# Kernel tuning notes

Hardware: AMD Instinct MI355X
Metric: run time of the kernel (lower is better)

## Reference

```python
import jax, jax.numpy as jnp
import numpy as np

EPS = 1e-5

def conv3x3(x, w, b, stride=1):
    y = jax.lax.conv_general_dilated(x, w, (stride, stride), 'SAME',
                                     dimension_numbers=('NCHW', 'OIHW', 'NCHW'))
    return y + b[None, :, None, None]

def batchnorm_train(x, gamma, beta):
    # training-mode BN: batch statistics over (N, H, W)
    mean = x.mean(axis=(0, 2, 3), keepdims=True)
    var = x.var(axis=(0, 2, 3), keepdims=True)
    xh = (x - mean) * jax.lax.rsqrt(var + EPS)
    return xh * gamma[None, :, None, None] + beta[None, :, None, None]

def haar_dwt2(x):
    # pywt.dwt2(x, 'db1') on last two axes; even H,W so 'symmetric' padding is a no-op.
    # a = (x0 + x1)/sqrt2, d = (x0 - x1)/sqrt2 per axis -> 2x2 block combinations / 2.
    x00 = x[:, :, 0::2, 0::2]
    x01 = x[:, :, 0::2, 1::2]
    x10 = x[:, :, 1::2, 0::2]
    x11 = x[:, :, 1::2, 1::2]
    cA = (x00 + x01 + x10 + x11) * 0.5
    cH = (x00 + x01 - x10 - x11) * 0.5  # pywt 'da': detail along rows
    cV = (x00 - x01 + x10 - x11) * 0.5  # pywt 'ad': detail along cols
    cD = (x00 - x01 - x10 + x11) * 0.5
    return cA, cH, cV, cD


def setup_inputs() -> dict:
    key = jax.random.key(0)
    ks = jax.random.split(key, 8)
    N, in_c, out_c, H, W = 4, 3, 64, 512, 512

    def kaiming(k, shape):
        fan_in = shape[1] * shape[2] * shape[3]
        return jax.random.normal(k, shape, jnp.float32) * np.sqrt(2.0 / fan_in)

    inputs = jax.random.normal(ks[0], (N, in_c, H, W), jnp.float32)
    return {
        'inputs': inputs,
        # conv_block: conv1 -> bn1 -> conv2 -> bn2 -> relu
        'w1': kaiming(ks[1], (out_c, in_c, 3, 3)),
        'b1': jnp.zeros((out_c,), jnp.float32),
        'g1': jnp.ones((out_c,), jnp.float32),
        'be1': jnp.zeros((out_c,), jnp.float32),
        'w2': kaiming(ks[2], (out_c, out_c, 3, 3)),
        'b2': jnp.zeros((out_c,), jnp.float32),
        'g2': jnp.ones((out_c,), jnp.float32),
        'be2': jnp.zeros((out_c,), jnp.float32),
        # conv_dwt_block: conv(out_c*4 -> out_c) -> bn -> relu
        'w3': kaiming(ks[3], (out_c, out_c * 4, 3, 3)),
        'b3': jnp.zeros((out_c,), jnp.float32),
        'g3': jnp.ones((out_c,), jnp.float32),
        'be3': jnp.zeros((out_c,), jnp.float32),
    }


def reference(inputs, w1, b1, g1, be1, w2, b2, g2, be2, w3, b3, g3, be3):
    # conv_block
    x = conv3x3(inputs, w1, b1)
    x = batchnorm_train(x, g1, be1)
    x = conv3x3(x, w2, b2)
    x = batchnorm_train(x, g2, be2)
    skip_con = jax.nn.relu(x)

    # original detaches skip_con before the (CPU pywt) DWT -> no grad through this branch
    dwt_in = jax.lax.stop_gradient(skip_con)
    cA, cH, cV, cD = haar_dwt2(dwt_in)
    dwt = jnp.concatenate((cA, cH, cV, cD), axis=1)  # [N, 4*out_c, H/2, W/2]

    y = conv3x3(dwt, w3, b3)
    y = batchnorm_train(y, g3, be3)
    dwt_out = jax.nn.relu(y)
    return dwt_out, skip_con
```

## Files before the change

### kernel.cpp

```cpp
#include <hip/hip_runtime.h>
#include <cstdint>

typedef float f32x4 __attribute__((ext_vector_type(4)));
typedef __bf16 bf16x8 __attribute__((ext_vector_type(8)));
typedef unsigned int uint32;
typedef unsigned short ushort_t;

__device__ __forceinline__ ushort_t f2bf(float f) {
    uint32 u = __builtin_bit_cast(uint32, f);
    u = (u + 0x7fffu + ((u >> 16) & 1u)) >> 16;
    return (ushort_t)u;
}
__device__ __forceinline__ float bf2f(ushort_t h) {
    return __builtin_bit_cast(float, (uint32)h << 16);
}

__global__ __launch_bounds__(256) void im2col1_kernel(
    const float* __restrict__ in,
    ushort_t* __restrict__ P)
{
    int px = blockIdx.x * 256 + threadIdx.x;
    int n = px >> 18, rem = px & 262143;
    int y = rem >> 9, x = rem & 511;
    ushort_t pv[32];
#pragma unroll
    for (int ci = 0; ci < 3; ++ci)
#pragma unroll
        for (int t = 0; t < 9; ++t) {
            int dy = t / 3 - 1, dx = t % 3 - 1;
            int yy = y + dy, xx = x + dx;
            bool v = ((unsigned)yy < 512u) && ((unsigned)xx < 512u);
            pv[ci * 9 + t] = v ? f2bf(in[((n * 3 + ci) * 512 + yy) * 512 + xx])
                               : (ushort_t)0;
        }
#pragma unroll
    for (int k = 27; k < 32; ++k) pv[k] = 0;
    uint4* dst = (uint4*)(P + (size_t)px * 32);
    dst[0] = *(uint4*)(pv);
    dst[1] = *(uint4*)(pv + 8);
    dst[2] = *(uint4*)(pv + 16);
    dst[3] = *(uint4*)(pv + 24);
}

__global__ void prepw1_kernel(const float* __restrict__ w1,
                              ushort_t* __restrict__ Wsw1)
{
    int i = blockIdx.x * 256 + threadIdx.x;
    int ii = i & 7, lane = (i >> 3) & 63, nt = i >> 9;
    int cout = nt * 16 + (lane & 15);
    int k = (lane >> 4) * 8 + ii;
    Wsw1[i] = (k < 27) ? f2bf(w1[cout * 27 + k]) : (ushort_t)0;
}

__global__ __launch_bounds__(256) void gemm1_kernel(
    const ushort_t* __restrict__ P,
    const ushort_t* __restrict__ Wsw1,
    const float* __restrict__ b1,
    ushort_t* __restrict__ X1,
    float* __restrict__ stats)
{
    __shared__ float sred[4][128];
    int tid = threadIdx.x;
    int wave = tid >> 6, lane = tid & 63;
    int lp = lane & 15, lg = lane >> 4;
    int pxb = blockIdx.x * 256 + wave * 64;

    bf16x8 wf[4];
#pragma unroll
    for (int nt = 0; nt < 4; ++nt)
        wf[nt] = *(const bf16x8*)(Wsw1 + (nt * 64 + lane) * 8);

    f32x4 acc[4][4];
#pragma unroll
    for (int a = 0; a < 4; ++a)
#pragma unroll
        for (int b = 0; b < 4; ++b) acc[a][b] = (f32x4){0.f, 0.f, 0.f, 0.f};

#pragma unroll
    for (int nf = 0; nf < 4; ++nf) {
        bf16x8 bfrag = *(const bf16x8*)(P + (size_t)(pxb + nf * 16 + lp) * 32 + lg * 8);
#pragma unroll
        for (int nt = 0; nt < 4; ++nt)
            acc[nt][nf] = __builtin_amdgcn_mfma_f32_16x16x32_bf16(
                wf[nt], bfrag, acc[nt][nf], 0, 0, 0);
    }

    float s16[16], q16[16];
#pragma unroll
    for (int j = 0; j < 16; ++j) { s16[j] = 0.f; q16[j] = 0.f; }

#pragma unroll
    for (int nf = 0; nf < 4; ++nf) {
        size_t px = (size_t)pxb + nf * 16 + lp;
#pragma unroll
        for (int nt = 0; nt < 4; ++nt) {
            ushort_t ov[4];
#pragma unroll
            for (int r = 0; r < 4; ++r) {
                float o = acc[nt][nf][r] + b1[nt * 16 + lg * 4 + r];
                s16[nt * 4 + r] += o;
                q16[nt * 4 + r] += o * o;
                ov[r] = f2bf(o);
            }
            *(ushort4*)(X1 + px * 64 + nt * 16 + lg * 4) = *(ushort4*)ov;
        }
    }

#pragma unroll
    for (int off = 1; off < 16; off <<= 1)
#pragma unroll
        for (int j = 0; j < 16; ++j) {
            s16[j] += __shfl_xor(s16[j], off);
            q16[j] += __shfl_xor(q16[j], off);
        }
    if (lp == 0) {
#pragma unroll
        for (int nt = 0; nt < 4; ++nt)
#pragma unroll
            for (int r = 0; r < 4; ++r) {
                int ch = nt * 16 + lg * 4 + r;
                sred[wave][ch]      = s16[nt * 4 + r];
                sred[wave][64 + ch] = q16[nt * 4 + r];
            }
    }
    __syncthreads();
    if (tid < 128) {
        float tot = sred[0][tid] + sred[1][tid] + sred[2][tid] + sred[3][tid];
        atomicAdd(&stats[(blockIdx.x & 31) * 128 + tid], tot);
    }
}

__global__ void finalize_kernel(const float* __restrict__ stats,
                                const float* __restrict__ gamma,
                                const float* __restrict__ beta,
                                float inv_cnt, float* __restrict__ scsh)
{
    int c = threadIdx.x;
    float S = 0.f, Q = 0.f;
    for (int b = 0; b < 32; ++b) {
        S += stats[b * 128 + c];
        Q += stats[b * 128 + 64 + c];
    }
    float mean = S * inv_cnt;
    float var  = Q * inv_cnt - mean * mean;
    float rs   = rsqrtf(var + 1e-5f);
    float sc   = gamma[c] * rs;
    scsh[c]      = sc;
    scsh[64 + c] = beta[c] - mean * sc;
}

__global__ __launch_bounds__(256) void prepw_kernel(
    const float* __restrict__ w, const float* __restrict__ scale,
    ushort_t* __restrict__ Wsw, int CIN)
{
    int i = blockIdx.x * 256 + threadIdx.x;
    int KC = CIN >> 5;
    int ii = i & 7, lane = (i >> 3) & 63, nt = (i >> 9) & 3;
    int rest = i >> 11;
    int kc = rest % KC, t = rest / KC;
    if (t >= 9) return;
    int cout = nt * 16 + (lane & 15);
    int cin  = kc * 32 + (lane >> 4) * 8 + ii;
    float v = w[(cout * CIN + cin) * 9 + t];
    if (scale) v *= scale[cin];
    Wsw[i] = f2bf(v);
}

__global__ void prepT_kernel(const float* __restrict__ w2,
                             const float* __restrict__ shift,
                             float* __restrict__ T)
{
    int idx = threadIdx.x;
    if (idx < 576) {
        int t = idx / 64, cout = idx % 64;
        float s = 0.f;
        for (int cin = 0; cin < 64; ++cin)
            s += w2[(cout * 64 + cin) * 9 + t] * shift[cin];
        T[idx] = s;
    }
    __syncthreads();
    if (idx < 64) {
        float s = 0.f;
        for (int t = 0; t < 9; ++t) s += T[t * 64 + idx];
        T[576 + idx] = s;
    }
}

template <int CIN, bool HAS_T, int HH, int WW>
__global__ __launch_bounds__(256, 4) void conv_mfma4_kernel(
    const ushort_t* __restrict__ X,
    const ushort_t* __restrict__ Wsw,
    const float* __restrict__ T,
    const float* __restrict__ bias,
    ushort_t* __restrict__ Y,
    float* __restrict__ stats)
{
    constexpr int KC     = CIN >> 5;
    constexpr int COLS_B = WW >> 6;
    constexpr int ROWS_B = HH >> 2;

    __shared__ ushort_t tile[12672];
    __shared__ float sred[4][128];

    int nwg = gridDim.x;
    int bid = blockIdx.x;
    int cpx = nwg >> 3;
    int bs  = (bid & 7) * cpx + (bid >> 3);

    int tid  = threadIdx.x;
    int wave = tid >> 6, lane = tid & 63;
    int lp = lane & 15, lg = lane >> 4;

    int tmp = bs;
    int ctile = tmp % COLS_B;  tmp /= COLS_B;
    int rtile = tmp % ROWS_B;
    int n     = tmp / ROWS_B;
    int y0 = rtile << 2, x0 = ctile << 6;
    int y  = y0 + wave;

    f32x4 acc[4][4];
#pragma unroll
    for (int a = 0; a < 4; ++a)
#pragma unroll
        for (int b = 0; b < 4; ++b) acc[a][b] = (f32x4){0.f, 0.f, 0.f, 0.f};

#pragma unroll 1
    for (int c = 0; c < KC; ++c) {
        if (c) __syncthreads();
#pragma unroll
        for (int j = 0; j < 7; ++j) {
            int s = tid + j * 256;
            if (s < 1584) {
                int px = s >> 2, cb = s & 3;
                int ry = px / 66, cx = px - ry * 66;
                int gy = y0 - 1 + ry, gx = x0 - 1 + cx;
                uint4 v = {0u, 0u, 0u, 0u};
                if (((unsigned)gy < (unsigned)HH) && ((unsigned)gx < (unsigned)WW))
                    v = *(const uint4*)(X + ((size_t)(n * HH + gy) * WW + gx) * CIN
                                          + c * 32 + cb * 8);
                *(uint4*)(tile + cb * 3168 + px * 8) = v;
            }
        }
        __syncthreads();

#pragma unroll
        for (int t = 0; t < 9; ++t) {
            const int dy = t / 3 - 1, dx = t % 3 - 1;
            bf16x8 wf[4];
#pragma unroll
            for (int nt = 0; nt < 4; ++nt)
                wf[nt] = *(const bf16x8*)(Wsw + (size_t)(((t * KC + c) << 2) + nt) * 512 + lane * 8);
            int prow = (wave + 1 + dy) * 66 + (1 + dx) + lp;
#pragma unroll
            for (int nf = 0; nf < 4; ++nf) {
                int px = prow + nf * 16;
                bf16x8 bfrag = *(const bf16x8*)(tile + lg * 3168 + px * 8);
#pragma unroll
                for (int nt = 0; nt < 4; ++nt)
                    acc[nt][nf] = __builtin_amdgcn_mfma_f32_16x16x32_bf16(
                        wf[nt], bfrag, acc[nt][nf], 0, 0, 0);
            }
        }
    }

    bool top = (y == 0), bot = (y == HH - 1);
    float s16[16], q16[16];
#pragma unroll
    for (int j = 0; j < 16; ++j) { s16[j] = 0.f; q16[j] = 0.f; }

    size_t rowbase = ((size_t)(n * HH + y) * WW) * 64;
#pragma unroll
    for (int nf = 0; nf < 4; ++nf) {
        int x = x0 + nf * 16 + lp;
        bool lft = (x == 0), rgt = (x == WW - 1);
        bool edge = top | bot | lft | rgt;
#pragma unroll
        for (int nt = 0; nt < 4; ++nt) {
            ushort_t ov[4];
#pragma unroll
            for (int r = 0; r < 4; ++r) {
                int ch = nt * 16 + lg * 4 + r;
                float o = acc[nt][nf][r] + bias[ch];
                if (HAS_T) {
                    o += T[576 + ch];
                    if (edge) {
#pragma unroll
                        for (int t = 0; t < 9; ++t) {
                            int dy = t / 3 - 1, dx = t % 3 - 1;
                            bool miss = (top && dy < 0) || (bot && dy > 0) ||
                                        (lft && dx < 0) || (rgt && dx > 0);
                            if (miss) o -= T[t * 64 + ch];
                        }
                    }
                }
                s16[nt * 4 + r] += o;
                q16[nt * 4 + r] += o * o;
                ov[r] = f2bf(o);
            }
            *(ushort4*)(Y + rowbase + (size_t)x * 64 + nt * 16 + lg * 4) = *(ushort4*)ov;
        }
    }

#pragma unroll
    for (int off = 1; off < 16; off <<= 1)
#pragma unroll
        for (int j = 0; j < 16; ++j) {
            s16[j] += __shfl_xor(s16[j], off);
            q16[j] += __shfl_xor(q16[j], off);
        }
    if (lp == 0) {
#pragma unroll
        for (int nt = 0; nt < 4; ++nt)
#pragma unroll
            for (int r = 0; r < 4; ++r) {
                int ch = nt * 16 + lg * 4 + r;
                sred[wave][ch]      = s16[nt * 4 + r];
                sred[wave][64 + ch] = q16[nt * 4 + r];
            }
    }
    __syncthreads();
    if (tid < 128) {
        float tot = sred[0][tid] + sred[1][tid] + sred[2][tid] + sred[3][tid];
        atomicAdd(&stats[(bs & 31) * 128 + tid], tot);
    }
}

__global__ __launch_bounds__(256) void bn2_dwt_skip_kernel(
    const ushort_t* __restrict__ X2, const float* __restrict__ scsh,
    float* __restrict__ skip,
    ushort_t* __restrict__ X3)
{
    __shared__ float v[128][65];
    int tid = threadIdx.x;
    int b = blockIdx.x;
    int n  = b >> 11;
    int r2 = b & 2047;
    int y0 = (r2 >> 3) << 1;
    int x0 = (r2 & 7) << 6;

#pragma unroll
    for (int k = 0; k < 4; ++k) {
        int q  = tid + k * 256;
        int px = q >> 3;
        int cb = (q & 7) * 8;
        int gy = y0 + (px >> 6);
        int gx = x0 + (px & 63);
        uint4 raw = *(const uint4*)(X2 + ((size_t)(n * 512 + gy) * 512 + gx) * 64 + cb);
        const ushort_t* up = (const ushort_t*)&raw;
#pragma unroll
        for (int j = 0; j < 8; ++j) {
            float f = bf2f(up[j]);
            float o = f * scsh[cb + j] + scsh[64 + cb + j];
            v[px][cb + j] = fmaxf(o, 0.f);
        }
    }
    __syncthreads();

    {
        int c = tid >> 2, sub = tid & 3;
#pragma unroll
        for (int rr = 0; rr < 2; ++rr) {
            float* orow = skip + ((size_t)(n * 64 + c) * 512 + (y0 + rr)) * 512 + x0;
#pragma unroll
            for (int qq = 0; qq < 4; ++qq) {
                int xb = qq * 16 + sub * 4;
                float4 w4;
                w4.x = v[rr * 64 + xb + 0][c];
                w4.y = v[rr * 64 + xb + 1][c];
                w4.z = v[rr * 64 + xb + 2][c];
                w4.w = v[rr * 64 + xb + 3][c];
                *(float4*)(orow + xb) = w4;
            }
        }
    }
    {
        int c = tid & 63, jj = tid >> 6;
        int yq = y0 >> 1, xq = x0 >> 1;
#pragma unroll
        for (int it = 0; it < 8; ++it) {
            int xl = jj * 8 + it;
            float x00 = v[2 * xl][c],      x01 = v[2 * xl + 1][c];
            float x10 = v[64 + 2 * xl][c], x11 = v[64 + 2 * xl + 1][c];
            float cA = (x00 + x01 + x10 + x11) * 0.5f;
            float cH = (x00 + x01 - x10 - x11) * 0.5f;
            float cV = (x00 - x01 + x10 - x11) * 0.5f;
            float cD = (x00 - x01 - x10 + x11) * 0.5f;
            ushort_t* dst = X3 + ((size_t)(n * 256 + yq) * 256 + xq + xl) * 256 + c;
            dst[0]   = f2bf(cA);
            dst[64]  = f2bf(cH);
            dst[128] = f2bf(cV);
            dst[192] = f2bf(cD);
        }
    }
}

__global__ __launch_bounds__(256) void bn3_kernel(
    const ushort_t* __restrict__ X4, const float* __restrict__ scsh,
    float* __restrict__ out)
{
    __shared__ float v[64][65];
    int tid = threadIdx.x;
    int b = blockIdx.x;
    int n  = b >> 10;
    int r2 = b & 1023;
    int y  = r2 >> 2;
    int x0 = (r2 & 3) << 6;

#pragma unroll
    for (int k = 0; k < 2; ++k) {
        int q  = tid + k * 256;
        int px = q >> 3;
        int cb = (q & 7) * 8;
        uint4 raw = *(const uint4*)(X4 + ((size_t)(n * 256 + y) * 256 + x0 + px) * 64 + cb);
        const ushort_t* up = (const ushort_t*)&raw;
#pragma unroll
        for (int j = 0; j < 8; ++j) {
            float f = bf2f(up[j]);
            float o = f * scsh[cb + j] + scsh[64 + cb + j];
            v[px][cb + j] = fmaxf(o, 0.f);
        }
    }
    __syncthreads();
    int c = tid >> 2, sub = tid & 3;
    float* orow = out + ((size_t)(n * 64 + c) * 256 + y) * 256 + x0;
#pragma unroll
    for (int qq = 0; qq < 4; ++qq) {
        int xb = qq * 16 + sub * 4;
        float4 w4;
        w4.x = v[xb + 0][c];
        w4.y = v[xb + 1][c];
        w4.z = v[xb + 2][c];
        w4.w = v[xb + 3][c];
        *(float4*)(orow + xb) = w4;
    }
}

extern "C" void kernel_launch(void* const* d_in, const int* in_sizes, int n_in,
                              void* d_out, int out_size, void* d_ws, size_t ws_size,
                              hipStream_t stream)
{
    const float* in  = (const float*)d_in[0];
    const float* w1  = (const float*)d_in[1];
    const float* b1  = (const float*)d_in[2];
    const float* g1  = (const float*)d_in[3];
    const float* be1 = (const float*)d_in[4];
    const float* w2  = (const float*)d_in[5];
    const float* b2  = (const float*)d_in[6];
    const float* g2  = (const float*)d_in[7];
    const float* be2 = (const float*)d_in[8];
    const float* w3  = (const float*)d_in[9];
    const float* b3  = (const float*)d_in[10];
    const float* g3  = (const float*)d_in[11];
    const float* be3 = (const float*)d_in[12];

    float* out     = (float*)d_out;
    float* dwt_out = out;
    float* skip    = out + 16777216;

    char* ws = (char*)d_ws;
    ushort_t* X1 = (ushort_t*)ws;
    ushort_t* X2 = (ushort_t*)(ws + 134217728);
    ushort_t* P  = X2;
    ushort_t* X3 = X1;
    ushort_t* X4 = X2;
    char* aux = ws + 268435456;
    float* stats1 = (float*)(aux);
    float* stats2 = (float*)(aux + 16384);
    float* stats3 = (float*)(aux + 32768);
    float* scsh1  = (float*)(aux + 49152);
    float* scsh2  = (float*)(aux + 49664);
    float* scsh3  = (float*)(aux + 50176);
    float* T2     = (float*)(aux + 50688);
    ushort_t* Wsw2 = (ushort_t*)(aux + 57344);
    ushort_t* Wsw3 = (ushort_t*)(aux + 131072);
    ushort_t* Wsw1 = (ushort_t*)(aux + 425984);

    hipMemsetAsync(aux, 0, 49152, stream);

    im2col1_kernel<<<4096, 256, 0, stream>>>(in, P);
    prepw1_kernel<<<8, 256, 0, stream>>>(w1, Wsw1);
    gemm1_kernel<<<4096, 256, 0, stream>>>(P, Wsw1, b1, X1, stats1);
    finalize_kernel<<<1, 64, 0, stream>>>(stats1, g1, be1, 1.f / 1048576.f, scsh1);
    prepw_kernel<<<144, 256, 0, stream>>>(w2, scsh1, Wsw2, 64);
    prepT_kernel<<<1, 576, 0, stream>>>(w2, scsh1 + 64, T2);

    conv_mfma4_kernel<64, true, 512, 512><<<4096, 256, 0, stream>>>(
        X1, Wsw2, T2, b2, X2, stats2);
    finalize_kernel<<<1, 64, 0, stream>>>(stats2, g2, be2, 1.f / 1048576.f, scsh2);

    bn2_dwt_skip_kernel<<<8192, 256, 0, stream>>>(X2, scsh2, skip, X3);

    prepw_kernel<<<576, 256, 0, stream>>>(w3, nullptr, Wsw3, 256);
    conv_mfma4_kernel<256, false, 256, 256><<<1024, 256, 0, stream>>>(
        X3, Wsw3, nullptr, b3, X4, stats3);
    finalize_kernel<<<1, 64, 0, stream>>>(stats3, g3, be3, 1.f / 262144.f, scsh3);

    bn3_kernel<<<4096, 256, 0, stream>>>(X4, scsh3, dwt_out);
}
```

Before: 552.9 us.

## Double-buffer conv input tiles with direct global-to-LDS async loads

Replaces the register-staged global-to-LDS tile copy in the implicit-GEMM conv with global_load_lds direct copies into two LDS buffers. The next channel chunk is prefetched while MFMAs run on the current one, and the two barriers per iteration become one. Global offsets and boundary masks are precomputed once, and the halo zeros are written to both buffers up front. LDS use doubles and occupancy drops from 4 to 3 blocks. The 64-channel conv2 has only two chunks, so it gets little overlap.

```diff
diff --git a/kernel.cpp b/kernel.cpp
--- a/kernel.cpp
+++ b/kernel.cpp
@@ -13,6 +13,12 @@
 }
 __device__ __forceinline__ float bf2f(ushort_t h) {
     return __builtin_bit_cast(float, (uint32)h << 16);
+}
+
+__device__ __forceinline__ void gload_lds16(const void* g, void* l) {
+    __builtin_amdgcn_global_load_lds(
+        (const __attribute__((address_space(1))) uint32*)g,
+        (__attribute__((address_space(3))) uint32*)l, 16, 0, 0);
 }
 
 __global__ __launch_bounds__(256) void im2col1_kernel(
@@ -187,7 +193,7 @@
 }
 
 template <int CIN, bool HAS_T, int HH, int WW>
-__global__ __launch_bounds__(256, 4) void conv_mfma4_kernel(
+__global__ __launch_bounds__(256, 3) void conv_mfma5_kernel(
     const ushort_t* __restrict__ X,
     const ushort_t* __restrict__ Wsw,
     const float* __restrict__ T,
@@ -199,8 +205,7 @@
     constexpr int COLS_B = WW >> 6;
     constexpr int ROWS_B = HH >> 2;
 
-    __shared__ ushort_t tile[12672];
-    __shared__ float sred[4][128];
+    __shared__ ushort_t tiles[2][12672];
 
     int nwg = gridDim.x;
     int bid = blockIdx.x;
@@ -218,30 +223,54 @@
     int y0 = rtile << 2, x0 = ctile << 6;
     int y  = y0 + wave;
 
+    uint32 goff[7];
+    uint32 vmask = 0;
+#pragma unroll
+    for (int j = 0; j < 7; ++j) {
+        int s = tid + j * 256;
+        goff[j] = 0;
+        if (s < 1584) {
+            int plane = s / 396;
+            int px    = s - plane * 396;
+            int ry    = px / 66;
+            int cx    = px - ry * 66;
+            int gy = y0 - 1 + ry, gx = x0 - 1 + cx;
+            if (((unsigned)gy < (unsigned)HH) && ((unsigned)gx < (unsigned)WW)) {
+                vmask |= (1u << j);
+                goff[j] = (uint32)((((uint32)(n * HH + gy) * WW + gx) * CIN
+                                    + plane * 8) * 2);
+            } else {
+                uint4 zz; zz.x = zz.y = zz.z = zz.w = 0u;
+                *(uint4*)((char*)tiles[0] + s * 16) = zz;
+                *(uint4*)((char*)tiles[1] + s * 16) = zz;
+            }
+        }
+    }
+
+    const char* Xb = (const char*)X;
+    auto stage = [&](int c, int b) {
+        uint32 cofs = (uint32)c * 64u;
+#pragma unroll
+        for (int j = 0; j < 7; ++j) {
+            if (vmask & (1u << j))
+                gload_lds16(Xb + goff[j] + cofs,
+                            (char*)tiles[b] + j * 4096 + wave * 1024);
+        }
+    };
+
     f32x4 acc[4][4];
 #pragma unroll
     for (int a = 0; a < 4; ++a)
 #pragma unroll
         for (int b = 0; b < 4; ++b) acc[a][b] = (f32x4){0.f, 0.f, 0.f, 0.f};
+
+    stage(0, 0);
+    __syncthreads();
 
 #pragma unroll 1
     for (int c = 0; c < KC; ++c) {
-        if (c) __syncthreads();
-#pragma unroll
-        for (int j = 0; j < 7; ++j) {
-            int s = tid + j * 256;
-            if (s < 1584) {
-                int px = s >> 2, cb = s & 3;
-                int ry = px / 66, cx = px - ry * 66;
-                int gy = y0 - 1 + ry, gx = x0 - 1 + cx;
-                uint4 v = {0u, 0u, 0u, 0u};
-                if (((unsigned)gy < (unsigned)HH) && ((unsigned)gx < (unsigned)WW))
-                    v = *(const uint4*)(X + ((size_t)(n * HH + gy) * WW + gx) * CIN
-                                          + c * 32 + cb * 8);
-                *(uint4*)(tile + cb * 3168 + px * 8) = v;
-            }
-        }
-        __syncthreads();
+        if (c + 1 < KC) stage(c + 1, (c + 1) & 1);
+        const ushort_t* tile = tiles[c & 1];
 
 #pragma unroll
         for (int t = 0; t < 9; ++t) {
@@ -261,7 +290,10 @@
                         wf[nt], bfrag, acc[nt][nf], 0, 0, 0);
             }
         }
-    }
+        __syncthreads();
+    }
+
+    float (*sred)[128] = (float(*)[128])tiles[0];
 
     bool top = (y == 0), bot = (y == HH - 1);
     float s16[16], q16[16];
@@ -484,14 +516,14 @@
     prepw_kernel<<<144, 256, 0, stream>>>(w2, scsh1, Wsw2, 64);
     prepT_kernel<<<1, 576, 0, stream>>>(w2, scsh1 + 64, T2);
 
-    conv_mfma4_kernel<64, true, 512, 512><<<4096, 256, 0, stream>>>(
+    conv_mfma5_kernel<64, true, 512, 512><<<4096, 256, 0, stream>>>(
         X1, Wsw2, T2, b2, X2, stats2);
     finalize_kernel<<<1, 64, 0, stream>>>(stats2, g2, be2, 1.f / 1048576.f, scsh2);
 
     bn2_dwt_skip_kernel<<<8192, 256, 0, stream>>>(X2, scsh2, skip, X3);
 
     prepw_kernel<<<576, 256, 0, stream>>>(w3, nullptr, Wsw3, 256);
-    conv_mfma4_kernel<256, false, 256, 256><<<1024, 256, 0, stream>>>(
+    conv_mfma5_kernel<256, false, 256, 256><<<1024, 256, 0, stream>>>(
         X3, Wsw3, nullptr, b3, X4, stats3);
     finalize_kernel<<<1, 64, 0, stream>>>(stats3, g3, be3, 1.f / 262144.f, scsh3);
 
```

New measurement: 594.1 us. +7.5%, slower.

## Use zero-padded channel-planar activations and read conv operands directly from global

Applied to the files above, without the earlier changes.

Intermediate activations are stored in a zero-padded, 32-channel-plane layout whose halo is cleared by a new pad kernel. The producer kernels (gemm1 via an LDS staging buffer, and the DWT) write into this padded layout. The conv kernels drop the LDS tile staging and its barriers and load MFMA B fragments directly from global memory/cache with no bounds checks. Weight packing is reordered to match a sequential pointer walk. This removes the LDS copy and syncs, but relies on L1/L2 to absorb the 9x reuse of each input and adds workspace and padding writes.

```diff
diff --git a/kernel.cpp b/kernel.cpp
--- a/kernel.cpp
+++ b/kernel.cpp
@@ -13,6 +13,23 @@
 }
 __device__ __forceinline__ float bf2f(ushort_t h) {
     return __builtin_bit_cast(float, (uint32)h << 16);
+}
+
+__global__ __launch_bounds__(256) void pad_zero_kernel(
+    char* __restrict__ p, int nplanes, int PH, int PW)
+{
+    int per = 2 * PW + 2 * (PH - 2);
+    int total = nplanes * per;
+    uint4 z = {0u, 0u, 0u, 0u};
+    for (int i = blockIdx.x * 256 + threadIdx.x; i < total; i += gridDim.x * 256) {
+        int pl = i / per, r = i - pl * per;
+        int y, x;
+        if (r < PW)            { y = 0;      x = r; }
+        else if (r < 2 * PW)   { y = PH - 1; x = r - PW; }
+        else { int q = r - 2 * PW; y = 1 + (q >> 1); x = (q & 1) ? (PW - 1) : 0; }
+        uint4* dst = (uint4*)(p + ((size_t)(pl * PH + y) * PW + x) * 64);
+        dst[0] = z; dst[1] = z; dst[2] = z; dst[3] = z;
+    }
 }
 
 __global__ __launch_bounds__(256) void im2col1_kernel(
@@ -56,14 +73,16 @@
     const ushort_t* __restrict__ P,
     const ushort_t* __restrict__ Wsw1,
     const float* __restrict__ b1,
-    ushort_t* __restrict__ X1,
+    ushort_t* __restrict__ X1p,
     float* __restrict__ stats)
 {
+    __shared__ ushort_t obuf[2][256][32];
     __shared__ float sred[4][128];
     int tid = threadIdx.x;
     int wave = tid >> 6, lane = tid & 63;
     int lp = lane & 15, lg = lane >> 4;
-    int pxb = blockIdx.x * 256 + wave * 64;
+    int pxb0 = blockIdx.x * 256;
+    int pxb = pxb0 + wave * 64;
 
     bf16x8 wf[4];
 #pragma unroll
@@ -91,18 +110,17 @@
 
 #pragma unroll
     for (int nf = 0; nf < 4; ++nf) {
-        size_t px = (size_t)pxb + nf * 16 + lp;
+        int pxl = wave * 64 + nf * 16 + lp;
 #pragma unroll
         for (int nt = 0; nt < 4; ++nt) {
-            ushort_t ov[4];
 #pragma unroll
             for (int r = 0; r < 4; ++r) {
-                float o = acc[nt][nf][r] + b1[nt * 16 + lg * 4 + r];
+                int ch = nt * 16 + lg * 4 + r;
+                float o = acc[nt][nf][r] + b1[ch];
                 s16[nt * 4 + r] += o;
                 q16[nt * 4 + r] += o * o;
-                ov[r] = f2bf(o);
-            }
-            *(ushort4*)(X1 + px * 64 + nt * 16 + lg * 4) = *(ushort4*)ov;
+                obuf[ch >> 5][pxl][ch & 31] = f2bf(o);
+            }
         }
     }
 
@@ -127,6 +145,19 @@
     if (tid < 128) {
         float tot = sred[0][tid] + sred[1][tid] + sred[2][tid] + sred[3][tid];
         atomicAdd(&stats[(blockIdx.x & 31) * 128 + tid], tot);
+    }
+    int n  = pxb0 >> 18;
+    int y  = (pxb0 >> 9) & 511;
+    int x0 = pxb0 & 511;
+#pragma unroll
+    for (int k = 0; k < 8; ++k) {
+        int idx = tid + k * 256;
+        int cpl = idx >> 10;
+        int pxl = (idx >> 2) & 255;
+        int q   = idx & 3;
+        uint4 v = *(uint4*)&obuf[cpl][pxl][q * 8];
+        *(uint4*)(X1p + (((size_t)(n * 2 + cpl) * 514 + y + 1) * 514 + x0 + pxl + 1) * 32
+                      + q * 8) = v;
     }
 }
 
@@ -157,8 +188,8 @@
     int KC = CIN >> 5;
     int ii = i & 7, lane = (i >> 3) & 63, nt = (i >> 9) & 3;
     int rest = i >> 11;
-    int kc = rest % KC, t = rest / KC;
-    if (t >= 9) return;
+    if (rest >= 9 * KC) return;
+    int t = rest % 9, kc = rest / 9;
     int cout = nt * 16 + (lane & 15);
     int cin  = kc * 32 + (lane >> 4) * 8 + ii;
     float v = w[(cout * CIN + cin) * 9 + t];
@@ -187,36 +218,41 @@
 }
 
 template <int CIN, bool HAS_T, int HH, int WW>
-__global__ __launch_bounds__(256, 4) void conv_mfma4_kernel(
-    const ushort_t* __restrict__ X,
+__global__ __launch_bounds__(256, 4) void conv_mfma8_kernel(
+    const ushort_t* __restrict__ Xp,
     const ushort_t* __restrict__ Wsw,
     const float* __restrict__ T,
     const float* __restrict__ bias,
     ushort_t* __restrict__ Y,
     float* __restrict__ stats)
 {
-    constexpr int KC     = CIN >> 5;
-    constexpr int COLS_B = WW >> 6;
-    constexpr int ROWS_B = HH >> 2;
-
-    __shared__ ushort_t tile[12672];
+    constexpr int KC = CIN >> 5;
+    constexpr int PW = WW + 2, PH = HH + 2;
+    constexpr size_t PLANE = (size_t)PH * PW * 64;
+    constexpr int COLS_B = WW >> 6, ROWS_B = HH >> 2;
+
     __shared__ float sred[4][128];
 
-    int nwg = gridDim.x;
-    int bid = blockIdx.x;
-    int cpx = nwg >> 3;
-    int bs  = (bid & 7) * cpx + (bid >> 3);
-
-    int tid  = threadIdx.x;
-    int wave = tid >> 6, lane = tid & 63;
+    int nwg = gridDim.x, bid = blockIdx.x, cpx = nwg >> 3;
+    int bs = (bid & 7) * cpx + (bid >> 3);
+
+    int tid = threadIdx.x, wave = tid >> 6, lane = tid & 63;
     int lp = lane & 15, lg = lane >> 4;
 
     int tmp = bs;
-    int ctile = tmp % COLS_B;  tmp /= COLS_B;
+    int ctile = tmp % COLS_B; tmp /= COLS_B;
     int rtile = tmp % ROWS_B;
-    int n     = tmp / ROWS_B;
+    int n = tmp / ROWS_B;
     int y0 = rtile << 2, x0 = ctile << 6;
-    int y  = y0 + wave;
+    int y = y0 + wave;
+
+    const char* rb[3];
+#pragma unroll
+    for (int d = 0; d < 3; ++d)
+        rb[d] = (const char*)Xp
+              + (((size_t)n * KC * PH + (y + d)) * PW + x0 + lp) * 64 + lg * 16;
+
+    const char* wp = (const char*)Wsw + lane * 16;
 
     f32x4 acc[4][4];
 #pragma unroll
@@ -226,41 +262,25 @@
 
 #pragma unroll 1
     for (int c = 0; c < KC; ++c) {
-        if (c) __syncthreads();
-#pragma unroll
-        for (int j = 0; j < 7; ++j) {
-            int s = tid + j * 256;
-            if (s < 1584) {
-                int px = s >> 2, cb = s & 3;
-                int ry = px / 66, cx = px - ry * 66;
-                int gy = y0 - 1 + ry, gx = x0 - 1 + cx;
-                uint4 v = {0u, 0u, 0u, 0u};
-                if (((unsigned)gy < (unsigned)HH) && ((unsigned)gx < (unsigned)WW))
-                    v = *(const uint4*)(X + ((size_t)(n * HH + gy) * WW + gx) * CIN
-                                          + c * 32 + cb * 8);
-                *(uint4*)(tile + cb * 3168 + px * 8) = v;
-            }
-        }
-        __syncthreads();
-
 #pragma unroll
         for (int t = 0; t < 9; ++t) {
-            const int dy = t / 3 - 1, dx = t % 3 - 1;
+            const int dyi = t / 3, dxi = t % 3;
             bf16x8 wf[4];
 #pragma unroll
             for (int nt = 0; nt < 4; ++nt)
-                wf[nt] = *(const bf16x8*)(Wsw + (size_t)(((t * KC + c) << 2) + nt) * 512 + lane * 8);
-            int prow = (wave + 1 + dy) * 66 + (1 + dx) + lp;
+                wf[nt] = *(const bf16x8*)(wp + nt * 1024);
 #pragma unroll
             for (int nf = 0; nf < 4; ++nf) {
-                int px = prow + nf * 16;
-                bf16x8 bfrag = *(const bf16x8*)(tile + lg * 3168 + px * 8);
+                bf16x8 bfrag = *(const bf16x8*)(rb[dyi] + (dxi + nf * 16) * 64);
 #pragma unroll
                 for (int nt = 0; nt < 4; ++nt)
                     acc[nt][nf] = __builtin_amdgcn_mfma_f32_16x16x32_bf16(
                         wf[nt], bfrag, acc[nt][nf], 0, 0, 0);
             }
-        }
+            wp += 4096;
+        }
+#pragma unroll
+        for (int d = 0; d < 3; ++d) rb[d] += PLANE;
     }
 
     bool top = (y == 0), bot = (y == HH - 1);
@@ -328,7 +348,7 @@
 __global__ __launch_bounds__(256) void bn2_dwt_skip_kernel(
     const ushort_t* __restrict__ X2, const float* __restrict__ scsh,
     float* __restrict__ skip,
-    ushort_t* __restrict__ X3)
+    ushort_t* __restrict__ X3p)
 {
     __shared__ float v[128][65];
     int tid = threadIdx.x;
@@ -376,6 +396,7 @@
     {
         int c = tid & 63, jj = tid >> 6;
         int yq = y0 >> 1, xq = x0 >> 1;
+        int coff = c & 31, chk = c >> 5;
 #pragma unroll
         for (int it = 0; it < 8; ++it) {
             int xl = jj * 8 + it;
@@ -385,11 +406,13 @@
             float cH = (x00 + x01 - x10 - x11) * 0.5f;
             float cV = (x00 - x01 + x10 - x11) * 0.5f;
             float cD = (x00 - x01 - x10 + x11) * 0.5f;
-            ushort_t* dst = X3 + ((size_t)(n * 256 + yq) * 256 + xq + xl) * 256 + c;
-            dst[0]   = f2bf(cA);
-            dst[64]  = f2bf(cH);
-            dst[128] = f2bf(cV);
-            dst[192] = f2bf(cD);
+            float vals[4] = {cA, cH, cV, cD};
+#pragma unroll
+            for (int kb = 0; kb < 4; ++kb) {
+                int plane = n * 8 + kb * 2 + chk;
+                X3p[(((size_t)plane * 258 + yq + 1) * 258 + xq + xl + 1) * 32 + coff]
+                    = f2bf(vals[kb]);
+            }
         }
     }
 }
@@ -458,12 +481,12 @@
     float* skip    = out + 16777216;
 
     char* ws = (char*)d_ws;
-    ushort_t* X1 = (ushort_t*)ws;
-    ushort_t* X2 = (ushort_t*)(ws + 134217728);
-    ushort_t* P  = X2;
-    ushort_t* X3 = X1;
-    ushort_t* X4 = X2;
-    char* aux = ws + 268435456;
+    ushort_t* X1p = (ushort_t*)(ws);
+    ushort_t* X2  = (ushort_t*)(ws + 135268352);
+    ushort_t* X3p = (ushort_t*)(ws + 269486080);
+    ushort_t* X4  = (ushort_t*)(ws + 405809152);
+    ushort_t* P   = (ushort_t*)(ws + 439363584);
+    char* aux = ws + 506472448;
     float* stats1 = (float*)(aux);
     float* stats2 = (float*)(aux + 16384);
     float* stats3 = (float*)(aux + 32768);
@@ -477,22 +500,25 @@
 
     hipMemsetAsync(aux, 0, 49152, stream);
 
+    pad_zero_kernel<<<64, 256, 0, stream>>>((char*)X1p, 8, 514, 514);
+    pad_zero_kernel<<<128, 256, 0, stream>>>((char*)X3p, 32, 258, 258);
+
     im2col1_kernel<<<4096, 256, 0, stream>>>(in, P);
     prepw1_kernel<<<8, 256, 0, stream>>>(w1, Wsw1);
-    gemm1_kernel<<<4096, 256, 0, stream>>>(P, Wsw1, b1, X1, stats1);
+    gemm1_kernel<<<4096, 256, 0, stream>>>(P, Wsw1, b1, X1p, stats1);
     finalize_kernel<<<1, 64, 0, stream>>>(stats1, g1, be1, 1.f / 1048576.f, scsh1);
     prepw_kernel<<<144, 256, 0, stream>>>(w2, scsh1, Wsw2, 64);
     prepT_kernel<<<1, 576, 0, stream>>>(w2, scsh1 + 64, T2);
 
-    conv_mfma4_kernel<64, true, 512, 512><<<4096, 256, 0, stream>>>(
-        X1, Wsw2, T2, b2, X2, stats2);
+    conv_mfma8_kernel<64, true, 512, 512><<<4096, 256, 0, stream>>>(
+        X1p, Wsw2, T2, b2, X2, stats2);
     finalize_kernel<<<1, 64, 0, stream>>>(stats2, g2, be2, 1.f / 1048576.f, scsh2);
 
-    bn2_dwt_skip_kernel<<<8192, 256, 0, stream>>>(X2, scsh2, skip, X3);
+    bn2_dwt_skip_kernel<<<8192, 256, 0, stream>>>(X2, scsh2, skip, X3p);
 
     prepw_kernel<<<576, 256, 0, stream>>>(w3, nullptr, Wsw3, 256);
-    conv_mfma4_kernel<256, false, 256, 256><<<1024, 256, 0, stream>>>(
-        X3, Wsw3, nullptr, b3, X4, stats3);
+    conv_mfma8_kernel<256, false, 256, 256><<<1024, 256, 0, stream>>>(
+        X3p, Wsw3, nullptr, b3, X4, stats3);
     finalize_kernel<<<1, 64, 0, stream>>>(stats3, g3, be3, 1.f / 262144.f, scsh3);
 
     bn3_kernel<<<4096, 256, 0, stream>>>(X4, scsh3, dwt_out);
```

Measured after the change: 679.1 us. 1.23x slower.

## Widen conv tiles to 128 columns with XOR-swizzled LDS layout

Applied to the files above, without the earlier changes.

Each conv workgroup now covers 4 rows by 128 columns instead of 64, doubling the MFMA accumulators per wave so each weight fragment load is reused across twice as many pixels and halo overhead per tile shrinks. The LDS tile is changed from channel-block planes to a per-pixel 64-byte layout with an XOR swizzle to avoid bank conflicts on the fragment reads. The weight layout is reordered so the taps for one channel chunk sit next to each other. In exchange, register pressure rises (launch bounds drop to 2 blocks per SIMD), LDS use roughly doubles, and the grid halves, which lowers occupancy.

```diff
diff --git a/kernel.cpp b/kernel.cpp
--- a/kernel.cpp
+++ b/kernel.cpp
@@ -157,8 +157,8 @@
     int KC = CIN >> 5;
     int ii = i & 7, lane = (i >> 3) & 63, nt = (i >> 9) & 3;
     int rest = i >> 11;
-    int kc = rest % KC, t = rest / KC;
-    if (t >= 9) return;
+    if (rest >= 9 * KC) return;
+    int t = rest % 9, kc = rest / 9;
     int cout = nt * 16 + (lane & 15);
     int cin  = kc * 32 + (lane >> 4) * 8 + ii;
     float v = w[(cout * CIN + cin) * 9 + t];
@@ -187,7 +187,7 @@
 }
 
 template <int CIN, bool HAS_T, int HH, int WW>
-__global__ __launch_bounds__(256, 4) void conv_mfma4_kernel(
+__global__ __launch_bounds__(256, 2) void conv_mfma10_kernel(
     const ushort_t* __restrict__ X,
     const ushort_t* __restrict__ Wsw,
     const float* __restrict__ T,
@@ -196,49 +196,47 @@
     float* __restrict__ stats)
 {
     constexpr int KC     = CIN >> 5;
-    constexpr int COLS_B = WW >> 6;
+    constexpr int COLS_B = WW >> 7;
     constexpr int ROWS_B = HH >> 2;
-
-    __shared__ ushort_t tile[12672];
+    constexpr int NLD    = 3120;
+
+    __shared__ ushort_t tile[24960];
     __shared__ float sred[4][128];
 
-    int nwg = gridDim.x;
-    int bid = blockIdx.x;
-    int cpx = nwg >> 3;
-    int bs  = (bid & 7) * cpx + (bid >> 3);
-
-    int tid  = threadIdx.x;
-    int wave = tid >> 6, lane = tid & 63;
+    int nwg = gridDim.x, bid = blockIdx.x, cpx = nwg >> 3;
+    int bs = (bid & 7) * cpx + (bid >> 3);
+
+    int tid = threadIdx.x, wave = tid >> 6, lane = tid & 63;
     int lp = lane & 15, lg = lane >> 4;
 
     int tmp = bs;
-    int ctile = tmp % COLS_B;  tmp /= COLS_B;
+    int ctile = tmp % COLS_B; tmp /= COLS_B;
     int rtile = tmp % ROWS_B;
-    int n     = tmp / ROWS_B;
-    int y0 = rtile << 2, x0 = ctile << 6;
-    int y  = y0 + wave;
-
-    f32x4 acc[4][4];
+    int n = tmp / ROWS_B;
+    int y0 = rtile << 2, x0 = ctile << 7;
+    int y = y0 + wave;
+
+    f32x4 acc[4][8];
 #pragma unroll
     for (int a = 0; a < 4; ++a)
 #pragma unroll
-        for (int b = 0; b < 4; ++b) acc[a][b] = (f32x4){0.f, 0.f, 0.f, 0.f};
+        for (int b = 0; b < 8; ++b) acc[a][b] = (f32x4){0.f, 0.f, 0.f, 0.f};
 
 #pragma unroll 1
     for (int c = 0; c < KC; ++c) {
         if (c) __syncthreads();
 #pragma unroll
-        for (int j = 0; j < 7; ++j) {
+        for (int j = 0; j < 13; ++j) {
             int s = tid + j * 256;
-            if (s < 1584) {
+            if (s < NLD) {
                 int px = s >> 2, cb = s & 3;
-                int ry = px / 66, cx = px - ry * 66;
+                int ry = px / 130, cx = px - ry * 130;
                 int gy = y0 - 1 + ry, gx = x0 - 1 + cx;
                 uint4 v = {0u, 0u, 0u, 0u};
                 if (((unsigned)gy < (unsigned)HH) && ((unsigned)gx < (unsigned)WW))
                     v = *(const uint4*)(X + ((size_t)(n * HH + gy) * WW + gx) * CIN
                                           + c * 32 + cb * 8);
-                *(uint4*)(tile + cb * 3168 + px * 8) = v;
+                *(uint4*)((char*)tile + px * 64 + ((cb * 16) ^ (((px >> 1) & 3) << 4))) = v;
             }
         }
         __syncthreads();
@@ -249,12 +247,14 @@
             bf16x8 wf[4];
 #pragma unroll
             for (int nt = 0; nt < 4; ++nt)
-                wf[nt] = *(const bf16x8*)(Wsw + (size_t)(((t * KC + c) << 2) + nt) * 512 + lane * 8);
-            int prow = (wave + 1 + dy) * 66 + (1 + dx) + lp;
-#pragma unroll
-            for (int nf = 0; nf < 4; ++nf) {
-                int px = prow + nf * 16;
-                bf16x8 bfrag = *(const bf16x8*)(tile + lg * 3168 + px * 8);
+                wf[nt] = *(const bf16x8*)(Wsw + (size_t)(((c * 9 + t) * 4 + nt) * 512)
+                                              + lane * 8);
+            int base = (wave + 1 + dy) * 130 + (1 + dx) + lp;
+#pragma unroll
+            for (int nf = 0; nf < 8; ++nf) {
+                int lpx = base + nf * 16;
+                bf16x8 bfrag = *(const bf16x8*)((const char*)tile + lpx * 64
+                                   + ((lg * 16) ^ (((lpx >> 1) & 3) << 4)));
 #pragma unroll
                 for (int nt = 0; nt < 4; ++nt)
                     acc[nt][nf] = __builtin_amdgcn_mfma_f32_16x16x32_bf16(
@@ -270,7 +270,7 @@
 
     size_t rowbase = ((size_t)(n * HH + y) * WW) * 64;
 #pragma unroll
-    for (int nf = 0; nf < 4; ++nf) {
+    for (int nf = 0; nf < 8; ++nf) {
         int x = x0 + nf * 16 + lp;
         bool lft = (x == 0), rgt = (x == WW - 1);
         bool edge = top | bot | lft | rgt;
@@ -484,14 +484,14 @@
     prepw_kernel<<<144, 256, 0, stream>>>(w2, scsh1, Wsw2, 64);
     prepT_kernel<<<1, 576, 0, stream>>>(w2, scsh1 + 64, T2);
 
-    conv_mfma4_kernel<64, true, 512, 512><<<4096, 256, 0, stream>>>(
+    conv_mfma10_kernel<64, true, 512, 512><<<2048, 256, 0, stream>>>(
         X1, Wsw2, T2, b2, X2, stats2);
     finalize_kernel<<<1, 64, 0, stream>>>(stats2, g2, be2, 1.f / 1048576.f, scsh2);
 
     bn2_dwt_skip_kernel<<<8192, 256, 0, stream>>>(X2, scsh2, skip, X3);
 
     prepw_kernel<<<576, 256, 0, stream>>>(w3, nullptr, Wsw3, 256);
-    conv_mfma4_kernel<256, false, 256, 256><<<1024, 256, 0, stream>>>(
+    conv_mfma10_kernel<256, false, 256, 256><<<512, 256, 0, stream>>>(
         X3, Wsw3, nullptr, b3, X4, stats3);
     finalize_kernel<<<1, 64, 0, stream>>>(stats3, g3, be3, 1.f / 262144.f, scsh3);
 
```

After: 623.3 us. 12.7% more time.
